# Optimization experiments

Hardware: AMD Instinct MI355X
Metric: run time of the kernel (lower is better)

The kernel has to match this reference:

```python
import jax, jax.numpy as jnp
import numpy as np

EMBED_DIM = 1024
NUM_HEADS = 16
HEAD_DIM = EMBED_DIM // NUM_HEADS
L, B, S = 2048, 2, 2048


def setup_inputs() -> dict:
    key = jax.random.key(0)
    kq, kk, kv = jax.random.split(key, 3)
    q = jax.random.normal(kq, (L, B, EMBED_DIM), dtype=jnp.float32)
    k = jax.random.normal(kk, (S, B, EMBED_DIM), dtype=jnp.float32)
    v = jax.random.normal(kv, (S, B, EMBED_DIM), dtype=jnp.float32)
    return {"q": q, "k": k, "v": v}


def reference(q, k, v):
    Lq, Bq, D = q.shape
    Sq = k.shape[0]
    scaling = HEAD_DIM ** -0.5
    # (L, B, D) -> (B*H, L, head_dim), matching reshape + transpose in torch
    qh = (q * scaling).reshape(Lq, Bq * NUM_HEADS, HEAD_DIM).transpose(1, 0, 2)
    kh = k.reshape(Sq, Bq * NUM_HEADS, HEAD_DIM).transpose(1, 0, 2)
    vh = v.reshape(Sq, Bq * NUM_HEADS, HEAD_DIM).transpose(1, 0, 2)
    # qk: (B*H, L, S) -- the full attention matrix the module materializes
    qk = jnp.einsum('ild,isd->ils', qh, kh)
    attn = jax.nn.softmax(qk, axis=-1)
    # dropout_p = 0.0 -> identity
    out = jnp.einsum('ils,isd->ild', attn, vh)  # (B*H, L, head_dim)
    out = out.transpose(1, 0, 2).reshape(Lq, Bq, D)
    return out
```

## Files before the change

kernel.cpp:

```cpp
#include <hip/hip_runtime.h>
#include <hip/hip_bf16.h>
#include <math.h>

typedef __bf16 bf16x8 __attribute__((ext_vector_type(8)));
typedef __bf16 bf16x4 __attribute__((ext_vector_type(4)));
typedef float  f32x4  __attribute__((ext_vector_type(4)));

constexpr int EMBED = 1024;
constexpr int NH    = 16;
constexpr int HD    = 64;
constexpr int LL    = 2048;
constexpr int BB    = 2;
constexpr int SSEQ  = 2048;

constexpr int BQ = 64;
constexpr int BK = 64;
constexpr int NT = SSEQ / BK;

constexpr size_t KW_ELEMS = (size_t)BB * NH * SSEQ * HD;

__device__ __forceinline__ void gload16(const void* g, void* l) {
  __builtin_amdgcn_global_load_lds((const __attribute__((address_space(1))) unsigned int*)g,
                                   (__attribute__((address_space(3))) unsigned int*)l, 16, 0, 0);
}

__device__ __forceinline__ float exp2_fast(float x) {
  float r;
  asm("v_exp_f32 %0, %1" : "=v"(r) : "v"(x));
  return r;
}

__global__ __launch_bounds__(256) void prep_kv(const float* __restrict__ Kg,
                                               const float* __restrict__ Vg,
                                               __hip_bfloat16* __restrict__ kw,
                                               __hip_bfloat16* __restrict__ vtw) {
  __shared__ char tsh[64 * 128];
  const int bid = blockIdx.x;
  if (bid < 2048) {
    const int idx = bid * 256 + threadIdx.x;
    const int e8 = idx & 127;
    const int t2 = idx >> 7;
    const int b  = t2 & 1;
    const int s  = t2 >> 1;
    const int h  = e8 >> 3;
    const int d8 = e8 & 7;
    const float* src = Kg + ((size_t)s * BB + b) * EMBED + e8 * 8;
    float4 a = *(const float4*)src;
    float4 c = *(const float4*)(src + 4);
    bf16x8 w;
    w[0] = (__bf16)a.x; w[1] = (__bf16)a.y; w[2] = (__bf16)a.z; w[3] = (__bf16)a.w;
    w[4] = (__bf16)c.x; w[5] = (__bf16)c.y; w[6] = (__bf16)c.z; w[7] = (__bf16)c.w;
    *(bf16x8*)(kw + (((size_t)(b * NH + h) * SSEQ + s) * HD + d8 * 8)) = w;
  } else {
    const int vb2 = bid - 2048;
    const int st  = vb2 & 31;
    const int bh  = vb2 >> 5;
    const int b   = bh >> 4;
    const int h   = bh & 15;
    const int t   = threadIdx.x;

    {
      const int r  = t >> 2;
      const int c0 = (t & 3) * 16;
      const float* src = Vg + ((size_t)(st * 64 + r) * BB + b) * EMBED + h * HD + c0;
      float4 x0 = *(const float4*)(src);
      float4 x1 = *(const float4*)(src + 4);
      float4 x2 = *(const float4*)(src + 8);
      float4 x3 = *(const float4*)(src + 12);
      bf16x8 w0, w1;
      w0[0] = (__bf16)x0.x; w0[1] = (__bf16)x0.y; w0[2] = (__bf16)x0.z; w0[3] = (__bf16)x0.w;
      w0[4] = (__bf16)x1.x; w0[5] = (__bf16)x1.y; w0[6] = (__bf16)x1.z; w0[7] = (__bf16)x1.w;
      w1[0] = (__bf16)x2.x; w1[1] = (__bf16)x2.y; w1[2] = (__bf16)x2.z; w1[3] = (__bf16)x2.w;
      w1[4] = (__bf16)x3.x; w1[5] = (__bf16)x3.y; w1[6] = (__bf16)x3.z; w1[7] = (__bf16)x3.w;
      const int colb = ((c0 + (r >> 3) * 16) & 63) * 2;
      char* rowp = tsh + r * 128;
      *(bf16x8*)(rowp + colb)      = w0;
      *(bf16x8*)(rowp + colb + 16) = w1;
    }
    __syncthreads();
    {
      const int d   = t >> 2;
      const int sc0 = (t & 3) * 16;
      bf16x8 o0, o1;
#pragma unroll
      for (int i = 0; i < 8; ++i) {
        const int s = sc0 + i;
        o0[i] = *(const __bf16*)(tsh + s * 128 + (((d + (s >> 3) * 16) & 63) * 2));
      }
#pragma unroll
      for (int i = 8; i < 16; ++i) {
        const int s = sc0 + i;
        o1[i - 8] = *(const __bf16*)(tsh + s * 128 + (((d + (s >> 3) * 16) & 63) * 2));
      }
      __hip_bfloat16* dst = vtw + ((size_t)(bh * HD + d)) * SSEQ + st * 64 + sc0;
      *(bf16x8*)(dst)     = o0;
      *(bf16x8*)(dst + 8) = o1;
    }
  }
}

__global__ __launch_bounds__(256) void sdpa_fwd(const float* __restrict__ Qg,
                                                const __hip_bfloat16* __restrict__ Kw,
                                                const __hip_bfloat16* __restrict__ VTw,
                                                float* __restrict__ Og) {
  __shared__ char sh[40960];
  char* kbuf = sh;
  char* vbuf = sh + 16384;
  char* psh  = sh + 32768;

  const int tid  = threadIdx.x;
  const int wv   = tid >> 6;
  const int lane = tid & 63;
  const int g    = lane >> 4;
  const int qc   = lane & 15;

  const int bh = blockIdx.y;
  const int bb = bh >> 4;
  const int hh = bh & 15;

  const size_t rstride = (size_t)BB * EMBED;
  const float* qb = Qg + (size_t)bb * EMBED + hh * HD;
  float*       ob = Og + (size_t)bb * EMBED + hh * HD;
  const char*  kwb = (const char*)(Kw + (size_t)bh * SSEQ * HD);
  const char*  vtb = (const char*)(VTw + (size_t)bh * HD * SSEQ);

  const int qrow0 = blockIdx.x * BQ + wv * 16;

  const int r0  = (wv * 2 + 0) * 8 + (lane >> 3);
  const int r1  = (wv * 2 + 1) * 8 + (lane >> 3);
  const int ch0 = (lane & 7) ^ (r0 & 7);
  const int ch1 = (lane & 7) ^ (r1 & 7);
  const char* kg0 = kwb + r0 * 128 + ch0 * 16;
  const char* kg1 = kwb + r1 * 128 + ch1 * 16;
  const char* vg0 = vtb + r0 * 4096 + ch0 * 16;
  const char* vg1 = vtb + r1 * 4096 + ch1 * 16;
  char* kd0 = kbuf + (wv * 2 + 0) * 1024;
  char* kd1 = kbuf + (wv * 2 + 1) * 1024;
  char* vd0 = vbuf + (wv * 2 + 0) * 1024;
  char* vd1 = vbuf + (wv * 2 + 1) * 1024;

#define STAGE(B, T)                                        \
  do {                                                     \
    gload16(kg0 + (size_t)(T) * 8192, kd0 + (B) * 8192);   \
    gload16(kg1 + (size_t)(T) * 8192, kd1 + (B) * 8192);   \
    gload16(vg0 + (size_t)(T) * 128,  vd0 + (B) * 8192);   \
    gload16(vg1 + (size_t)(T) * 128,  vd1 + (B) * 8192);   \
  } while (0)

  constexpr float QSC = 0.125f * 1.4426950408889634f;
  bf16x8 qf[2];
  {
    const float* qr = qb + (size_t)(qrow0 + qc) * rstride;
#pragma unroll
    for (int f = 0; f < 2; ++f) {
      const float* p = qr + f * 32 + g * 8;
      float4 a = *(const float4*)p;
      float4 c = *(const float4*)(p + 4);
      qf[f][0] = (__bf16)(a.x * QSC); qf[f][1] = (__bf16)(a.y * QSC);
      qf[f][2] = (__bf16)(a.z * QSC); qf[f][3] = (__bf16)(a.w * QSC);
      qf[f][4] = (__bf16)(c.x * QSC); qf[f][5] = (__bf16)(c.y * QSC);
      qf[f][6] = (__bf16)(c.z * QSC); qf[f][7] = (__bf16)(c.w * QSC);
    }
  }

  f32x4 acc[4];
#pragma unroll
  for (int nb = 0; nb < 4; ++nb) { acc[nb][0] = 0.f; acc[nb][1] = 0.f; acc[nb][2] = 0.f; acc[nb][3] = 0.f; }
  float m = -INFINITY;
  float l = 0.f;

  STAGE(0, 0);
  __syncthreads();
  int cur = 0;

  for (int t = 0; t < NT; ++t) {
    if (t + 1 < NT) STAGE(cur ^ 1, t + 1);

    const char* kb = kbuf + cur * 8192;
    const char* vb = vbuf + cur * 8192;
    const int sw = (qc & 7) << 4;

    f32x4 st[4];
    __builtin_amdgcn_s_setprio(1);
#pragma unroll
    for (int sb = 0; sb < 4; ++sb) {
      const int base = (sb * 16 + qc) * 128;
      bf16x8 k0 = *(const bf16x8*)(kb + base + ((g * 16)      ^ sw));
      bf16x8 k1 = *(const bf16x8*)(kb + base + ((64 + g * 16) ^ sw));
      f32x4 a; a[0] = 0.f; a[1] = 0.f; a[2] = 0.f; a[3] = 0.f;
      a = __builtin_amdgcn_mfma_f32_16x16x32_bf16(k0, qf[0], a, 0, 0, 0);
      a = __builtin_amdgcn_mfma_f32_16x16x32_bf16(k1, qf[1], a, 0, 0, 0);
      st[sb] = a;
    }
    __builtin_amdgcn_s_setprio(0);

    float mx;
    {
      float m0 = fmaxf(fmaxf(st[0][0], st[0][1]), fmaxf(st[0][2], st[0][3]));
      float m1 = fmaxf(fmaxf(st[1][0], st[1][1]), fmaxf(st[1][2], st[1][3]));
      float m2 = fmaxf(fmaxf(st[2][0], st[2][1]), fmaxf(st[2][2], st[2][3]));
      float m3 = fmaxf(fmaxf(st[3][0], st[3][1]), fmaxf(st[3][2], st[3][3]));
      mx = fmaxf(fmaxf(m0, m1), fmaxf(m2, m3));
    }
    mx = fmaxf(mx, __shfl_xor(mx, 16));
    mx = fmaxf(mx, __shfl_xor(mx, 32));

    if (!__all(mx - m <= 8.0f)) {
      const float mnew  = fmaxf(m, mx);
      const float alpha = exp2_fast(m - mnew);
      m = mnew;
      l *= alpha;
      float ar[4];
#pragma unroll
      for (int r2 = 0; r2 < 4; ++r2) ar[r2] = __shfl(alpha, g * 4 + r2);
#pragma unroll
      for (int nb = 0; nb < 4; ++nb)
#pragma unroll
        for (int r2 = 0; r2 < 4; ++r2) acc[nb][r2] *= ar[r2];
    }

    float rs = 0.f;
#pragma unroll
    for (int sb = 0; sb < 4; ++sb)
#pragma unroll
      for (int r2 = 0; r2 < 4; ++r2) {
        float p = exp2_fast(st[sb][r2] - m);
        st[sb][r2] = p;
        rs += p;
      }
    rs += __shfl_xor(rs, 16);
    rs += __shfl_xor(rs, 32);
    l += rs;

    {
      char* pw = psh + wv * 2048;
#pragma unroll
      for (int sb = 0; sb < 4; ++sb) {
        bf16x4 p4;
        p4[0] = (__bf16)st[sb][0]; p4[1] = (__bf16)st[sb][1];
        p4[2] = (__bf16)st[sb][2]; p4[3] = (__bf16)st[sb][3];
        *(bf16x4*)(pw + qc * 128 + ((sb * 32 + g * 8) ^ sw)) = p4;
      }
      asm volatile("s_waitcnt lgkmcnt(0)" ::: "memory");
    }

    {
      const char* pw = psh + wv * 2048;
      bf16x8 pa0 = *(const bf16x8*)(pw + qc * 128 + ((g * 16)      ^ sw));
      bf16x8 pa1 = *(const bf16x8*)(pw + qc * 128 + ((64 + g * 16) ^ sw));
      __builtin_amdgcn_s_setprio(1);
#pragma unroll
      for (int nb = 0; nb < 4; ++nb) {
        const int vbase = (nb * 16 + qc) * 128;
        bf16x8 v0f = *(const bf16x8*)(vb + vbase + ((g * 16)      ^ sw));
        bf16x8 v1f = *(const bf16x8*)(vb + vbase + ((64 + g * 16) ^ sw));
        acc[nb] = __builtin_amdgcn_mfma_f32_16x16x32_bf16(pa0, v0f, acc[nb], 0, 0, 0);
        acc[nb] = __builtin_amdgcn_mfma_f32_16x16x32_bf16(pa1, v1f, acc[nb], 0, 0, 0);
      }
      __builtin_amdgcn_s_setprio(0);
    }

    __syncthreads();
    cur ^= 1;
  }
#undef STAGE

  float linv[4];
#pragma unroll
  for (int r2 = 0; r2 < 4; ++r2) {
    float lr = __shfl(l, g * 4 + r2);
    linv[r2] = 1.0f / lr;
  }
#pragma unroll
  for (int nb = 0; nb < 4; ++nb)
#pragma unroll
    for (int r2 = 0; r2 < 4; ++r2) {
      const int row = qrow0 + g * 4 + r2;
      ob[(size_t)row * rstride + nb * 16 + qc] = acc[nb][r2] * linv[r2];
    }
}

extern "C" void kernel_launch(void* const* d_in, const int* in_sizes, int n_in,
                              void* d_out, int out_size, void* d_ws, size_t ws_size,
                              hipStream_t stream) {
  const float* q = (const float*)d_in[0];
  const float* k = (const float*)d_in[1];
  const float* v = (const float*)d_in[2];
  float* o = (float*)d_out;
  __hip_bfloat16* kw  = (__hip_bfloat16*)d_ws;
  __hip_bfloat16* vtw = kw + KW_ELEMS;

  prep_kv<<<dim3(3072), dim3(256), 0, stream>>>(k, v, kw, vtw);
  dim3 grid(LL / BQ, BB * NH);
  sdpa_fwd<<<grid, dim3(256), 0, stream>>>(q, kw, vtw, o);
}
```

Measured before the change: 154.5 us.

## Use 128-row query blocks with 8 waves, XCD-aware block mapping, and unrolled double buffer

Doubles the query tile to 128 rows per block with 512 threads, so each staged K/V tile is shared by 8 waves instead of 4 and each wave issues half as many async loads per stage. Blocks are remapped on a 1D grid so that all blocks of the same head land on the same XCD, which should improve L2 reuse of K/V. The main loop is unrolled by two with fixed buffer offsets, removing the cur toggle. Larger blocks halve the grid to 512 blocks and raise LDS per block, which may lower occupancy or leave some CUs idle.

Result: faster. 141.0 us (-8.8%).

```diff
diff --git a/kernel.cpp b/kernel.cpp
--- a/kernel.cpp
+++ b/kernel.cpp
@@ -13,7 +13,7 @@
 constexpr int BB    = 2;
 constexpr int SSEQ  = 2048;
 
-constexpr int BQ = 64;
+constexpr int BQ = 128;
 constexpr int BK = 64;
 constexpr int NT = SSEQ / BK;
 
@@ -58,7 +58,6 @@
     const int b   = bh >> 4;
     const int h   = bh & 15;
     const int t   = threadIdx.x;
-
     {
       const int r  = t >> 2;
       const int c0 = (t & 3) * 16;
@@ -99,11 +98,11 @@
   }
 }
 
-__global__ __launch_bounds__(256) void sdpa_fwd(const float* __restrict__ Qg,
+__global__ __launch_bounds__(512) void sdpa_fwd(const float* __restrict__ Qg,
                                                 const __hip_bfloat16* __restrict__ Kw,
                                                 const __hip_bfloat16* __restrict__ VTw,
                                                 float* __restrict__ Og) {
-  __shared__ char sh[40960];
+  __shared__ char sh[49152];
   char* kbuf = sh;
   char* vbuf = sh + 16384;
   char* psh  = sh + 32768;
@@ -114,43 +113,39 @@
   const int g    = lane >> 4;
   const int qc   = lane & 15;
 
-  const int bh = blockIdx.y;
-  const int bb = bh >> 4;
-  const int hh = bh & 15;
+  const int bid = blockIdx.x;
+  const int xcd = bid & 7;
+  const int rest = bid >> 3;
+  const int qb  = rest & 15;
+  const int bh  = ((rest >> 4) << 3) | xcd;
+  const int bb  = bh >> 4;
+  const int hh  = bh & 15;
 
   const size_t rstride = (size_t)BB * EMBED;
-  const float* qb = Qg + (size_t)bb * EMBED + hh * HD;
-  float*       ob = Og + (size_t)bb * EMBED + hh * HD;
+  const float* qb_ptr = Qg + (size_t)bb * EMBED + hh * HD;
+  float*       ob     = Og + (size_t)bb * EMBED + hh * HD;
   const char*  kwb = (const char*)(Kw + (size_t)bh * SSEQ * HD);
   const char*  vtb = (const char*)(VTw + (size_t)bh * HD * SSEQ);
 
-  const int qrow0 = blockIdx.x * BQ + wv * 16;
-
-  const int r0  = (wv * 2 + 0) * 8 + (lane >> 3);
-  const int r1  = (wv * 2 + 1) * 8 + (lane >> 3);
-  const int ch0 = (lane & 7) ^ (r0 & 7);
-  const int ch1 = (lane & 7) ^ (r1 & 7);
-  const char* kg0 = kwb + r0 * 128 + ch0 * 16;
-  const char* kg1 = kwb + r1 * 128 + ch1 * 16;
-  const char* vg0 = vtb + r0 * 4096 + ch0 * 16;
-  const char* vg1 = vtb + r1 * 4096 + ch1 * 16;
-  char* kd0 = kbuf + (wv * 2 + 0) * 1024;
-  char* kd1 = kbuf + (wv * 2 + 1) * 1024;
-  char* vd0 = vbuf + (wv * 2 + 0) * 1024;
-  char* vd1 = vbuf + (wv * 2 + 1) * 1024;
-
-#define STAGE(B, T)                                        \
-  do {                                                     \
-    gload16(kg0 + (size_t)(T) * 8192, kd0 + (B) * 8192);   \
-    gload16(kg1 + (size_t)(T) * 8192, kd1 + (B) * 8192);   \
-    gload16(vg0 + (size_t)(T) * 128,  vd0 + (B) * 8192);   \
-    gload16(vg1 + (size_t)(T) * 128,  vd1 + (B) * 8192);   \
+  const int qrow0 = qb * BQ + wv * 16;
+
+  const int rW = wv * 8 + (lane >> 3);
+  const int cW = (lane & 7) ^ (rW & 7);
+  const char* kgS = kwb + rW * 128 + cW * 16;
+  const char* vgS = vtb + (size_t)rW * 4096 + cW * 16;
+  char* kdS = kbuf + wv * 1024;
+  char* vdS = vbuf + wv * 1024;
+
+#define STAGE(B, T)                                       \
+  do {                                                    \
+    gload16(kgS + (size_t)(T) * 8192, kdS + (B) * 8192);  \
+    gload16(vgS + (size_t)(T) * 128,  vdS + (B) * 8192);  \
   } while (0)
 
   constexpr float QSC = 0.125f * 1.4426950408889634f;
   bf16x8 qf[2];
   {
-    const float* qr = qb + (size_t)(qrow0 + qc) * rstride;
+    const float* qr = qb_ptr + (size_t)(qrow0 + qc) * rstride;
 #pragma unroll
     for (int f = 0; f < 2; ++f) {
       const float* p = qr + f * 32 + g * 8;
@@ -169,101 +164,96 @@
   float m = -INFINITY;
   float l = 0.f;
 
+  const int sw = (qc & 7) << 4;
+  char* pw = psh + wv * 2048;
+
+#define TILE(KOFF, VOFF)                                                      \
+  do {                                                                        \
+    const char* kb = kbuf + (KOFF);                                           \
+    const char* vb = vbuf + (VOFF);                                           \
+    f32x4 st[4];                                                              \
+    __builtin_amdgcn_s_setprio(1);                                            \
+    _Pragma("unroll")                                                         \
+    for (int sb = 0; sb < 4; ++sb) {                                          \
+      const int base = (sb * 16 + qc) * 128;                                  \
+      bf16x8 k0 = *(const bf16x8*)(kb + base + ((g * 16)      ^ sw));         \
+      bf16x8 k1 = *(const bf16x8*)(kb + base + ((64 + g * 16) ^ sw));         \
+      f32x4 a; a[0] = 0.f; a[1] = 0.f; a[2] = 0.f; a[3] = 0.f;                \
+      a = __builtin_amdgcn_mfma_f32_16x16x32_bf16(k0, qf[0], a, 0, 0, 0);     \
+      a = __builtin_amdgcn_mfma_f32_16x16x32_bf16(k1, qf[1], a, 0, 0, 0);     \
+      st[sb] = a;                                                             \
+    }                                                                         \
+    __builtin_amdgcn_s_setprio(0);                                            \
+    float mx = fmaxf(fmaxf(fmaxf(st[0][0], st[0][1]), st[0][2]),              \
+                     fmaxf(fmaxf(st[0][3], st[1][0]), st[1][1]));             \
+    mx = fmaxf(mx, fmaxf(fmaxf(st[1][2], st[1][3]), st[2][0]));               \
+    mx = fmaxf(mx, fmaxf(fmaxf(st[2][1], st[2][2]), st[2][3]));               \
+    mx = fmaxf(mx, fmaxf(fmaxf(st[3][0], st[3][1]),                           \
+                         fmaxf(st[3][2], st[3][3])));                         \
+    mx = fmaxf(mx, __shfl_xor(mx, 16));                                       \
+    mx = fmaxf(mx, __shfl_xor(mx, 32));                                       \
+    if (!__all(mx - m <= 8.0f)) {                                             \
+      const float mnew  = fmaxf(m, mx);                                       \
+      const float alpha = exp2_fast(m - mnew);                                \
+      m = mnew;                                                               \
+      l *= alpha;                                                             \
+      float ar[4];                                                            \
+      _Pragma("unroll")                                                       \
+      for (int r2 = 0; r2 < 4; ++r2) ar[r2] = __shfl(alpha, g * 4 + r2);      \
+      _Pragma("unroll")                                                       \
+      for (int nb = 0; nb < 4; ++nb)                                          \
+        _Pragma("unroll")                                                     \
+        for (int r2 = 0; r2 < 4; ++r2) acc[nb][r2] *= ar[r2];                 \
+    }                                                                         \
+    float rs = 0.f;                                                           \
+    _Pragma("unroll")                                                         \
+    for (int sb = 0; sb < 4; ++sb)                                            \
+      _Pragma("unroll")                                                       \
+      for (int r2 = 0; r2 < 4; ++r2) {                                        \
+        float p = exp2_fast(st[sb][r2] - m);                                  \
+        st[sb][r2] = p;                                                       \
+        rs += p;                                                              \
+      }                                                                       \
+    rs += __shfl_xor(rs, 16);                                                 \
+    rs += __shfl_xor(rs, 32);                                                 \
+    l += rs;                                                                  \
+    _Pragma("unroll")                                                         \
+    for (int sb = 0; sb < 4; ++sb) {                                          \
+      bf16x4 p4;                                                              \
+      p4[0] = (__bf16)st[sb][0]; p4[1] = (__bf16)st[sb][1];                   \
+      p4[2] = (__bf16)st[sb][2]; p4[3] = (__bf16)st[sb][3];                   \
+      *(bf16x4*)(pw + qc * 128 + ((sb * 32 + g * 8) ^ sw)) = p4;              \
+    }                                                                         \
+    asm volatile("s_waitcnt lgkmcnt(0)" ::: "memory");                        \
+    {                                                                         \
+      bf16x8 pa0 = *(const bf16x8*)(pw + qc * 128 + ((g * 16)      ^ sw));    \
+      bf16x8 pa1 = *(const bf16x8*)(pw + qc * 128 + ((64 + g * 16) ^ sw));    \
+      __builtin_amdgcn_s_setprio(1);                                          \
+      _Pragma("unroll")                                                       \
+      for (int nb = 0; nb < 4; ++nb) {                                        \
+        const int vbase = (nb * 16 + qc) * 128;                               \
+        bf16x8 v0f = *(const bf16x8*)(vb + vbase + ((g * 16)      ^ sw));     \
+        bf16x8 v1f = *(const bf16x8*)(vb + vbase + ((64 + g * 16) ^ sw));     \
+        acc[nb] = __builtin_amdgcn_mfma_f32_16x16x32_bf16(pa0, v0f, acc[nb], 0, 0, 0); \
+        acc[nb] = __builtin_amdgcn_mfma_f32_16x16x32_bf16(pa1, v1f, acc[nb], 0, 0, 0); \
+      }                                                                       \
+      __builtin_amdgcn_s_setprio(0);                                          \
+    }                                                                         \
+  } while (0)
+
   STAGE(0, 0);
   __syncthreads();
-  int cur = 0;
-
-  for (int t = 0; t < NT; ++t) {
-    if (t + 1 < NT) STAGE(cur ^ 1, t + 1);
-
-    const char* kb = kbuf + cur * 8192;
-    const char* vb = vbuf + cur * 8192;
-    const int sw = (qc & 7) << 4;
-
-    f32x4 st[4];
-    __builtin_amdgcn_s_setprio(1);
-#pragma unroll
-    for (int sb = 0; sb < 4; ++sb) {
-      const int base = (sb * 16 + qc) * 128;
-      bf16x8 k0 = *(const bf16x8*)(kb + base + ((g * 16)      ^ sw));
-      bf16x8 k1 = *(const bf16x8*)(kb + base + ((64 + g * 16) ^ sw));
-      f32x4 a; a[0] = 0.f; a[1] = 0.f; a[2] = 0.f; a[3] = 0.f;
-      a = __builtin_amdgcn_mfma_f32_16x16x32_bf16(k0, qf[0], a, 0, 0, 0);
-      a = __builtin_amdgcn_mfma_f32_16x16x32_bf16(k1, qf[1], a, 0, 0, 0);
-      st[sb] = a;
-    }
-    __builtin_amdgcn_s_setprio(0);
-
-    float mx;
-    {
-      float m0 = fmaxf(fmaxf(st[0][0], st[0][1]), fmaxf(st[0][2], st[0][3]));
-      float m1 = fmaxf(fmaxf(st[1][0], st[1][1]), fmaxf(st[1][2], st[1][3]));
-      float m2 = fmaxf(fmaxf(st[2][0], st[2][1]), fmaxf(st[2][2], st[2][3]));
-      float m3 = fmaxf(fmaxf(st[3][0], st[3][1]), fmaxf(st[3][2], st[3][3]));
-      mx = fmaxf(fmaxf(m0, m1), fmaxf(m2, m3));
-    }
-    mx = fmaxf(mx, __shfl_xor(mx, 16));
-    mx = fmaxf(mx, __shfl_xor(mx, 32));
-
-    if (!__all(mx - m <= 8.0f)) {
-      const float mnew  = fmaxf(m, mx);
-      const float alpha = exp2_fast(m - mnew);
-      m = mnew;
-      l *= alpha;
-      float ar[4];
-#pragma unroll
-      for (int r2 = 0; r2 < 4; ++r2) ar[r2] = __shfl(alpha, g * 4 + r2);
-#pragma unroll
-      for (int nb = 0; nb < 4; ++nb)
-#pragma unroll
-        for (int r2 = 0; r2 < 4; ++r2) acc[nb][r2] *= ar[r2];
-    }
-
-    float rs = 0.f;
-#pragma unroll
-    for (int sb = 0; sb < 4; ++sb)
-#pragma unroll
-      for (int r2 = 0; r2 < 4; ++r2) {
-        float p = exp2_fast(st[sb][r2] - m);
-        st[sb][r2] = p;
-        rs += p;
-      }
-    rs += __shfl_xor(rs, 16);
-    rs += __shfl_xor(rs, 32);
-    l += rs;
-
-    {
-      char* pw = psh + wv * 2048;
-#pragma unroll
-      for (int sb = 0; sb < 4; ++sb) {
-        bf16x4 p4;
-        p4[0] = (__bf16)st[sb][0]; p4[1] = (__bf16)st[sb][1];
-        p4[2] = (__bf16)st[sb][2]; p4[3] = (__bf16)st[sb][3];
-        *(bf16x4*)(pw + qc * 128 + ((sb * 32 + g * 8) ^ sw)) = p4;
-      }
-      asm volatile("s_waitcnt lgkmcnt(0)" ::: "memory");
-    }
-
-    {
-      const char* pw = psh + wv * 2048;
-      bf16x8 pa0 = *(const bf16x8*)(pw + qc * 128 + ((g * 16)      ^ sw));
-      bf16x8 pa1 = *(const bf16x8*)(pw + qc * 128 + ((64 + g * 16) ^ sw));
-      __builtin_amdgcn_s_setprio(1);
-#pragma unroll
-      for (int nb = 0; nb < 4; ++nb) {
-        const int vbase = (nb * 16 + qc) * 128;
-        bf16x8 v0f = *(const bf16x8*)(vb + vbase + ((g * 16)      ^ sw));
-        bf16x8 v1f = *(const bf16x8*)(vb + vbase + ((64 + g * 16) ^ sw));
-        acc[nb] = __builtin_amdgcn_mfma_f32_16x16x32_bf16(pa0, v0f, acc[nb], 0, 0, 0);
-        acc[nb] = __builtin_amdgcn_mfma_f32_16x16x32_bf16(pa1, v1f, acc[nb], 0, 0, 0);
-      }
-      __builtin_amdgcn_s_setprio(0);
-    }
-
+
+  for (int t = 0; t < NT; t += 2) {
+    if (t + 1 < NT) STAGE(1, t + 1);
+    TILE(0, 0);
     __syncthreads();
-    cur ^= 1;
+    if (t + 2 < NT) STAGE(0, t + 2);
+    TILE(8192, 8192);
+    __syncthreads();
   }
 #undef STAGE
+#undef TILE
 
   float linv[4];
 #pragma unroll
@@ -291,6 +281,5 @@
   __hip_bfloat16* vtw = kw + KW_ELEMS;
 
   prep_kv<<<dim3(3072), dim3(256), 0, stream>>>(k, v, kw, vtw);
-  dim3 grid(LL / BQ, BB * NH);
-  sdpa_fwd<<<grid, dim3(256), 0, stream>>>(q, kw, vtw, o);
-}
+  sdpa_fwd<<<dim3(512), dim3(512), 0, stream>>>(q, kw, vtw, o);
+}
```
